# Performance work log

Hardware: AMD Instinct MI355X
Metric: run time of the kernel (lower is better)

The kernel has to match this reference:

```python
import jax, jax.numpy as jnp
import numpy as np

B, L, C = 2, 2048, 1024
H = 16
D = C // H  # 64
MAX_SCALE_MUL = float(np.log(100.0))
EPS = 1e-12


def setup_inputs() -> dict:
    key = jax.random.key(0)
    ks = jax.random.split(key, 6)
    x = jax.random.normal(ks[0], (B, L, C), dtype=jnp.float32)
    attn_bias = jax.random.normal(ks[1], (1, 1, L, L), dtype=jnp.float32) * 0.02
    W_qkv = jax.random.normal(ks[2], (3 * C, C), dtype=jnp.float32) * (1.0 / np.sqrt(C))
    q_bias = jnp.zeros((C,), dtype=jnp.float32)
    v_bias = jnp.zeros((C,), dtype=jnp.float32)
    scale_mul = jnp.full((1, H, 1, 1), np.log(4.0), dtype=jnp.float32)
    W_proj = jax.random.normal(ks[3], (C, C), dtype=jnp.float32) * (1.0 / np.sqrt(C))
    b_proj = jnp.zeros((C,), dtype=jnp.float32)
    return {"x": x, "attn_bias": attn_bias, "W_qkv": W_qkv, "q_bias": q_bias,
            "v_bias": v_bias, "scale_mul": scale_mul, "W_proj": W_proj, "b_proj": b_proj}


def _l2norm(t):
    # F.normalize(dim=-1): x / max(||x||_2, eps)
    n = jnp.sqrt(jnp.sum(t * t, axis=-1, keepdims=True))
    return t / jnp.maximum(n, EPS)


def reference(x, attn_bias, W_qkv, q_bias, v_bias, scale_mul, W_proj, b_proj):
    bias = jnp.concatenate([q_bias, jnp.zeros_like(q_bias), v_bias])  # (3C,)
    qkv = x @ W_qkv.T + bias                     # (B, L, 3C)
    qkv = qkv.reshape(B, L, 3, H, D)
    q, k, v = jnp.moveaxis(qkv, 2, 0)            # each (B, L, H, D)
    q = jnp.transpose(q, (0, 2, 1, 3))           # (B, H, L, D)
    k = jnp.transpose(k, (0, 2, 1, 3))
    v = jnp.transpose(v, (0, 2, 1, 3))
    # attn_l2_norm path: scale = 1, learned per-head scale clamped at log(100)
    sm = jnp.exp(jnp.minimum(scale_mul, MAX_SCALE_MUL))  # (1, H, 1, 1)
    q = _l2norm(q) * sm
    k = _l2norm(k)
    scores = jnp.einsum('bhqd,bhkd->bhqk', q, k) + attn_bias  # scale=1
    attn = jax.nn.softmax(scores, axis=-1)
    out = jnp.einsum('bhqk,bhkd->bhqd', attn, v)  # (B, H, L, D)
    out = jnp.transpose(out, (0, 2, 1, 3)).reshape(B, L, C)
    return out @ W_proj.T + b_proj
```

## Files before the change

### kernel.cpp

```cpp
#include <hip/hip_runtime.h>


typedef __bf16 bf16x8 __attribute__((ext_vector_type(8)));
typedef __bf16 bf16x4 __attribute__((ext_vector_type(4)));
typedef float  f32x4  __attribute__((ext_vector_type(4)));

#define BB 2
#define LL 2048
#define CC 1024
#define HH 16
#define DD 64
#define LOG2E 1.44269504088896f

__device__ __forceinline__ f32x4 mfma_16x16x32(bf16x8 a, bf16x8 b, f32x4 c) {
    return __builtin_amdgcn_mfma_f32_16x16x32_bf16(a, b, c, 0, 0, 0);
}

__device__ __forceinline__ void gload_lds16(const __bf16* g, __bf16* lds) {
    __builtin_amdgcn_global_load_lds(
        (const __attribute__((address_space(1))) unsigned int*)g,
        (__attribute__((address_space(3))) unsigned int*)lds,
        16, 0, 0);
}

__device__ __forceinline__ unsigned pk_bf16(float a, float b) {
    unsigned short ua = __builtin_bit_cast(unsigned short, (__bf16)a);
    unsigned short ub = __builtin_bit_cast(unsigned short, (__bf16)b);
    return (unsigned)ua | ((unsigned)ub << 16);
}

__global__ __launch_bounds__(256) void cvt_bf16_kernel(const float* __restrict__ in,
                                                       __bf16* __restrict__ out, int n4) {
    int i = blockIdx.x * 256 + threadIdx.x;
    if (i >= n4) return;
    float4 v = reinterpret_cast<const float4*>(in)[i];
    bf16x4 o;
    o[0] = (__bf16)v.x; o[1] = (__bf16)v.y; o[2] = (__bf16)v.z; o[3] = (__bf16)v.w;
    reinterpret_cast<bf16x4*>(out)[i] = o;
}

__global__ __launch_bounds__(256) void bias_prep_kernel(const float* __restrict__ bias,
                                                        __bf16* __restrict__ bias_bf) {
    __shared__ float wmax[4];
    const int l = blockIdx.x, tid = threadIdx.x;
    const int w = tid >> 6;
    float4 a = reinterpret_cast<const float4*>(bias + (size_t)l * 2048)[tid];
    float4 b = reinterpret_cast<const float4*>(bias + (size_t)l * 2048 + 1024)[tid];
    float m = fmaxf(fmaxf(fmaxf(a.x, a.y), fmaxf(a.z, a.w)),
                    fmaxf(fmaxf(b.x, b.y), fmaxf(b.z, b.w)));
#pragma unroll
    for (int off = 1; off < 64; off <<= 1) m = fmaxf(m, __shfl_xor(m, off, 64));
    if ((tid & 63) == 0) wmax[w] = m;
    __syncthreads();
    float M = fmaxf(fmaxf(wmax[0], wmax[1]), fmaxf(wmax[2], wmax[3]));
    bf16x4 o0, o1;
    o0[0] = (__bf16)(a.x - M); o0[1] = (__bf16)(a.y - M);
    o0[2] = (__bf16)(a.z - M); o0[3] = (__bf16)(a.w - M);
    o1[0] = (__bf16)(b.x - M); o1[1] = (__bf16)(b.y - M);
    o1[2] = (__bf16)(b.z - M); o1[3] = (__bf16)(b.w - M);
    reinterpret_cast<bf16x4*>(bias_bf + (size_t)l * 2048)[tid] = o0;
    reinterpret_cast<bf16x4*>(bias_bf + (size_t)l * 2048 + 1024)[tid] = o1;
}

template <int OUT_MODE>
__global__ __launch_bounds__(256) void gemm_bt_kernel(
    const __bf16* __restrict__ A, const __bf16* __restrict__ Bm,
    float* __restrict__ Cf, __bf16* __restrict__ Cb,
    const float* __restrict__ bias, int M, int N, int K) {
    __shared__ __bf16 As[128 * 64];
    __shared__ __bf16 Bs[128 * 64];
    const int tid = threadIdx.x;
    const int m0 = blockIdx.x * 128, n0 = blockIdx.y * 128;
    const int w  = tid >> 6, l = tid & 63;
    const int wr = (w >> 1) * 64, wc = (w & 1) * 64;
    const int lr = l & 15, lg = l >> 4;
    const int rmask = (lr & 7) << 4;
    f32x4 acc[4][4] = {};
    const int lrow = l >> 3;
    const int celem = (((l & 7) ^ lrow) << 3);

    for (int kt = 0; kt < K; kt += 64) {
        __syncthreads();
#pragma unroll
        for (int i = 0; i < 4; ++i) {
            const int row = w * 32 + i * 8;
            gload_lds16(A + (size_t)(m0 + row + lrow) * K + kt + celem, &As[row * 64]);
            gload_lds16(Bm + (size_t)(n0 + row + lrow) * K + kt + celem, &Bs[row * 64]);
        }
        asm volatile("s_waitcnt vmcnt(0)" ::: "memory");
        __syncthreads();
#pragma unroll
        for (int kk = 0; kk < 2; ++kk) {
            bf16x8 af[4], bfr[4];
#pragma unroll
            for (int m = 0; m < 4; ++m)
                af[m] = *reinterpret_cast<const bf16x8*>(
                    (char*)As + (wr + m * 16 + lr) * 128 + ((kk * 64 + lg * 16) ^ rmask));
#pragma unroll
            for (int n = 0; n < 4; ++n)
                bfr[n] = *reinterpret_cast<const bf16x8*>(
                    (char*)Bs + (wc + n * 16 + lr) * 128 + ((kk * 64 + lg * 16) ^ rmask));
#pragma unroll
            for (int m = 0; m < 4; ++m)
#pragma unroll
                for (int n = 0; n < 4; ++n)
                    acc[m][n] = mfma_16x16x32(af[m], bfr[n], acc[m][n]);
        }
    }
#pragma unroll
    for (int m = 0; m < 4; ++m) {
#pragma unroll
        for (int n = 0; n < 4; ++n) {
            const int row = m0 + wr + m * 16 + lg * 4;
            const int col = n0 + wc + n * 16 + lr;
#pragma unroll
            for (int r = 0; r < 4; ++r) {
                float v = acc[m][n][r];
                if (OUT_MODE == 0) {
                    Cb[(size_t)(row + r) * N + col] = (__bf16)v;
                } else {
                    Cf[(size_t)(row + r) * N + col] = v + bias[col];
                }
            }
        }
    }
}

__global__ __launch_bounds__(256) void qkv_norm_kernel(
    const __bf16* __restrict__ qkv, const float* __restrict__ q_bias,
    const float* __restrict__ v_bias, const float* __restrict__ scale_mul,
    __bf16* __restrict__ Q, __bf16* __restrict__ K, __bf16* __restrict__ V) {
    const int bl = blockIdx.x;
    const int tid = threadIdx.x;
    const int w = tid >> 6, d = tid & 63;
    const int b = bl >> 11, l = bl & 2047;
    for (int g = w; g < 48; g += 4) {
        const int s = g >> 4, h = g & 15;
        float v = (float)qkv[(size_t)bl * 3072 + g * 64 + d];
        if (s == 0) v += q_bias[h * 64 + d];
        if (s == 2) v += v_bias[h * 64 + d];
        if (s < 2) {
            float ss = v * v;
#pragma unroll
            for (int off = 1; off < 64; off <<= 1) ss += __shfl_xor(ss, off, 64);
            float nrm = sqrtf(ss);
            v = v / fmaxf(nrm, 1e-12f);
            if (s == 0) v *= __expf(fminf(scale_mul[h], 4.60517019f));
        }
        __bf16* dst = (s == 0) ? Q : ((s == 1) ? K : V);
        dst[((size_t)(b * 16 + h) * 2048 + l) * 64 + d] = (__bf16)v;
    }
}

__global__ __launch_bounds__(256) void v_transpose_kernel(const __bf16* __restrict__ Vin,
                                                          __bf16* __restrict__ Vt) {
    __shared__ __bf16 T[64][72];
    const int lb = blockIdx.x, bh = blockIdx.y;
    const int tid = threadIdx.x;
    const size_t base = (size_t)bh * LL * DD;
    const int row = tid >> 2, c = (tid & 3) * 16;
    {
        const __bf16* src = Vin + base + (size_t)(lb * 64 + row) * 64 + c;
        *reinterpret_cast<bf16x8*>(&T[row][c])     = *reinterpret_cast<const bf16x8*>(src);
        *reinterpret_cast<bf16x8*>(&T[row][c + 8]) = *reinterpret_cast<const bf16x8*>(src + 8);
    }
    __syncthreads();
    bf16x8 o0, o1;
#pragma unroll
    for (int j = 0; j < 8; ++j) {
        o0[j] = T[c + j][row];
        o1[j] = T[c + 8 + j][row];
    }
    __bf16* dst = Vt + base + (size_t)row * 2048 + lb * 64 + c;
    *reinterpret_cast<bf16x8*>(dst)     = o0;
    *reinterpret_cast<bf16x8*>(dst + 8) = o1;
}

__global__ __launch_bounds__(256) void attn_kernel(
    const __bf16* __restrict__ Q, const __bf16* __restrict__ K,
    const __bf16* __restrict__ Vt, const __bf16* __restrict__ bias_bf,
    const float* __restrict__ scale_mul, __bf16* __restrict__ Octx) {
    __shared__ __bf16 KVs[2][2][64 * 64];
    const int bh = blockIdx.x, qb = blockIdx.y;
    const int tid = threadIdx.x;
    const int w = tid >> 6, l = tid & 63;
    const int lr = l & 15, lg = l >> 4;
    const int rmask = (lr & 7) << 4;
    const int b = bh >> 4, h = bh & 15;
    const size_t base = (size_t)bh * LL * DD;
    const float smh = __expf(fminf(scale_mul[h], 4.60517019f));
    const float cexp = -smh * LOG2E;

    const int gq = qb * 64 + w * 16 + lr;
    bf16x8 qf[2];
    qf[0] = *reinterpret_cast<const bf16x8*>(Q + base + (size_t)gq * 64 + lg * 8);
    qf[1] = *reinterpret_cast<const bf16x8*>(Q + base + (size_t)gq * 64 + 32 + lg * 8);
    const __bf16* brow = bias_bf + (size_t)gq * 2048;

    const int lrow = l >> 3;
    const int celem = (((l & 7) ^ lrow) << 3);
    auto stage = [&](int buf, int kb) {
        __bf16* Kd = &KVs[buf][0][0];
        __bf16* Vd = &KVs[buf][1][0];
#pragma unroll
        for (int i = 0; i < 2; ++i) {
            const int row = w * 16 + i * 8;
            gload_lds16(K  + base + ((size_t)kb * 64 + row + lrow) * 64 + celem, Kd + row * 64);
            gload_lds16(Vt + base + (size_t)(row + lrow) * 2048 + kb * 64 + celem, Vd + row * 64);
        }
    };

    stage(0, 0);
    asm volatile("s_waitcnt vmcnt(0)" ::: "memory");

    f32x4 Oa[4] = {};
    float lsum = 0.f;
    int cur = 0;
    bf16x4 bcur[4];
#pragma unroll
    for (int t = 0; t < 4; ++t)
        bcur[t] = *reinterpret_cast<const bf16x4*>(brow + t * 16 + lg * 4);

    const int sAx = lr + ((lg & 1) << 5);
    const int sBx = sAx + 16;

    for (int kb = 0; kb < 32; ++kb) {
        __syncthreads();
        if (kb < 31) stage(cur ^ 1, kb + 1);
        bf16x4 bnext[4];
        if (kb < 31) {
#pragma unroll
            for (int t = 0; t < 4; ++t)
                bnext[t] = *reinterpret_cast<const bf16x4*>(brow + (kb + 1) * 64 + t * 16 + lg * 4);
        }

        const char* Kc = (const char*)KVs[cur][0];
        const char* Vc = (const char*)KVs[cur][1];

        f32x4 sa[4] = {};
#pragma unroll
        for (int t = 0; t < 4; ++t) {
            const char* kr = Kc + (t * 16 + lr) * 128;
            bf16x8 kf0 = *reinterpret_cast<const bf16x8*>(kr + ((lg * 16) ^ rmask));
            bf16x8 kf1 = *reinterpret_cast<const bf16x8*>(kr + ((64 + lg * 16) ^ rmask));
            sa[t] = mfma_16x16x32(kf0, qf[0], sa[t]);
            sa[t] = mfma_16x16x32(kf1, qf[1], sa[t]);
        }

        unsigned wv[4][2];
#pragma unroll
        for (int t = 0; t < 4; ++t) {
            float pv[4];
#pragma unroll
            for (int r = 0; r < 4; ++r) {
                float s = sa[t][r] + (float)bcur[t][r];
                pv[r] = exp2f(fmaf(s, LOG2E, cexp));
                lsum += pv[r];
            }
            wv[t][0] = pk_bf16(pv[0], pv[1]);
            wv[t][1] = pk_bf16(pv[2], pv[3]);
        }

        int e0  = __shfl((int)wv[0][0], sAx, 64), e1  = __shfl((int)wv[0][1], sAx, 64);
        int e2  = __shfl((int)wv[0][0], sBx, 64), e3  = __shfl((int)wv[0][1], sBx, 64);
        int e4  = __shfl((int)wv[1][0], sAx, 64), e5  = __shfl((int)wv[1][1], sAx, 64);
        int e6  = __shfl((int)wv[1][0], sBx, 64), e7  = __shfl((int)wv[1][1], sBx, 64);
        int e8  = __shfl((int)wv[2][0], sAx, 64), e9  = __shfl((int)wv[2][1], sAx, 64);
        int e10 = __shfl((int)wv[2][0], sBx, 64), e11 = __shfl((int)wv[2][1], sBx, 64);
        int e12 = __shfl((int)wv[3][0], sAx, 64), e13 = __shfl((int)wv[3][1], sAx, 64);
        int e14 = __shfl((int)wv[3][0], sBx, 64), e15 = __shfl((int)wv[3][1], sBx, 64);
        const bool hi2 = (lg & 2) != 0;
        union Upa { unsigned u[4]; bf16x8 v; } pa0, pa1;
        pa0.u[0] = hi2 ? (unsigned)e4  : (unsigned)e0;
        pa0.u[1] = hi2 ? (unsigned)e5  : (unsigned)e1;
        pa0.u[2] = hi2 ? (unsigned)e6  : (unsigned)e2;
        pa0.u[3] = hi2 ? (unsigned)e7  : (unsigned)e3;
        pa1.u[0] = hi2 ? (unsigned)e12 : (unsigned)e8;
        pa1.u[1] = hi2 ? (unsigned)e13 : (unsigned)e9;
        pa1.u[2] = hi2 ? (unsigned)e14 : (unsigned)e10;
        pa1.u[3] = hi2 ? (unsigned)e15 : (unsigned)e11;

#pragma unroll
        for (int t = 0; t < 4; ++t) {
            const char* vr = Vc + (t * 16 + lr) * 128;
            bf16x8 vf0 = *reinterpret_cast<const bf16x8*>(vr + ((lg * 16) ^ rmask));
            bf16x8 vf1 = *reinterpret_cast<const bf16x8*>(vr + ((64 + lg * 16) ^ rmask));
            Oa[t] = mfma_16x16x32(pa0.v, vf0, Oa[t]);
            Oa[t] = mfma_16x16x32(pa1.v, vf1, Oa[t]);
        }

        if (kb < 31) {
            asm volatile("s_waitcnt vmcnt(0)" ::: "memory");
#pragma unroll
            for (int t = 0; t < 4; ++t) bcur[t] = bnext[t];
        }
        cur ^= 1;
    }

    lsum += __shfl_xor(lsum, 16, 64);
    lsum += __shfl_xor(lsum, 32, 64);
    float inv[4];
#pragma unroll
    for (int r = 0; r < 4; ++r) inv[r] = 1.0f / __shfl(lsum, lg * 4 + r, 64);

#pragma unroll
    for (int t = 0; t < 4; ++t)
#pragma unroll
        for (int r = 0; r < 4; ++r) {
            const int row = qb * 64 + w * 16 + lg * 4 + r;
            float o = Oa[t][r] * inv[r];
            Octx[((size_t)(b * 2048 + row)) * 1024 + h * 64 + t * 16 + lr] = (__bf16)o;
        }
}

extern "C" void kernel_launch(void* const* d_in, const int* in_sizes, int n_in,
                              void* d_out, int out_size, void* d_ws, size_t ws_size,
                              hipStream_t stream) {
    const float* x         = (const float*)d_in[0];
    const float* attn_bias = (const float*)d_in[1];
    const float* W_qkv     = (const float*)d_in[2];
    const float* q_bias    = (const float*)d_in[3];
    const float* v_bias    = (const float*)d_in[4];
    const float* scale_mul = (const float*)d_in[5];
    const float* W_proj    = (const float*)d_in[6];
    const float* b_proj    = (const float*)d_in[7];
    float* out = (float*)d_out;

    char* ws = (char*)d_ws;
    size_t off = 0;
    auto alloc = [&](size_t bytes) {
        void* p = ws + off;
        off = (off + bytes + 255) & ~(size_t)255;
        return p;
    };
    __bf16* xb     = (__bf16*)alloc((size_t)4096 * 1024 * 2);
    __bf16* wqkvb  = (__bf16*)alloc((size_t)3072 * 1024 * 2);
    __bf16* wprojb = (__bf16*)alloc((size_t)1024 * 1024 * 2);
    __bf16* qkvb   = (__bf16*)alloc((size_t)4096 * 3072 * 2);
    __bf16* Qw     = (__bf16*)alloc((size_t)BB * HH * LL * DD * 2);
    __bf16* Kw     = (__bf16*)alloc((size_t)BB * HH * LL * DD * 2);
    __bf16* Vw     = (__bf16*)alloc((size_t)BB * HH * LL * DD * 2);
    __bf16* Oc     = (__bf16*)alloc((size_t)4096 * 1024 * 2);
    __bf16* bias_bf = qkvb;
    __bf16* Vt      = qkvb + (size_t)2048 * 2048;

    cvt_bf16_kernel<<<4096, 256, 0, stream>>>(x, xb, 4096 * 1024 / 4);
    cvt_bf16_kernel<<<3072, 256, 0, stream>>>(W_qkv, wqkvb, 3072 * 1024 / 4);
    cvt_bf16_kernel<<<1024, 256, 0, stream>>>(W_proj, wprojb, 1024 * 1024 / 4);

    gemm_bt_kernel<0><<<dim3(32, 24), 256, 0, stream>>>(
        xb, wqkvb, nullptr, qkvb, nullptr, 4096, 3072, 1024);

    qkv_norm_kernel<<<4096, 256, 0, stream>>>(qkvb, q_bias, v_bias, scale_mul, Qw, Kw, Vw);

    bias_prep_kernel<<<2048, 256, 0, stream>>>(attn_bias, bias_bf);
    v_transpose_kernel<<<dim3(32, 32), 256, 0, stream>>>(Vw, Vt);

    attn_kernel<<<dim3(32, 32), 256, 0, stream>>>(Qw, Kw, Vt, bias_bf, scale_mul, Oc);

    gemm_bt_kernel<1><<<dim3(32, 8), 256, 0, stream>>>(
        Oc, wprojb, out, nullptr, b_proj, 4096, 1024, 1024);
}
```

Measured before the change: 200.5 us.

## Load K/V fragments directly from global and pass P through LDS

Drops the double-buffered LDS staging of K and V tiles along with the block barriers. Each wave now loads its K and V MFMA fragments straight from global memory, relying on L2/cache reuse across waves and blocks. The P transpose no longer uses 16 cross-lane shuffles; it is written to a small per-wave swizzled LDS tile and read back. The change also remaps block indices with a swizzle for better L2 locality and adds a launch_bounds occupancy hint. The risk is redundant global traffic, since each of the four waves fetches the same K/V, and exposed global-load latency without explicit prefetch.

```diff
diff --git a/kernel.cpp b/kernel.cpp
--- a/kernel.cpp
+++ b/kernel.cpp
@@ -21,12 +21,6 @@
         (const __attribute__((address_space(1))) unsigned int*)g,
         (__attribute__((address_space(3))) unsigned int*)lds,
         16, 0, 0);
-}
-
-__device__ __forceinline__ unsigned pk_bf16(float a, float b) {
-    unsigned short ua = __builtin_bit_cast(unsigned short, (__bf16)a);
-    unsigned short ub = __builtin_bit_cast(unsigned short, (__bf16)b);
-    return (unsigned)ua | ((unsigned)ub << 16);
 }
 
 __global__ __launch_bounds__(256) void cvt_bf16_kernel(const float* __restrict__ in,
@@ -176,13 +170,15 @@
     *reinterpret_cast<bf16x8*>(dst + 8) = o1;
 }
 
-__global__ __launch_bounds__(256) void attn_kernel(
+__global__ __launch_bounds__(256, 4) void attn_kernel(
     const __bf16* __restrict__ Q, const __bf16* __restrict__ K,
     const __bf16* __restrict__ Vt, const __bf16* __restrict__ bias_bf,
     const float* __restrict__ scale_mul, __bf16* __restrict__ Octx) {
-    __shared__ __bf16 KVs[2][2][64 * 64];
-    const int bh = blockIdx.x, qb = blockIdx.y;
+    __shared__ __bf16 Ps[64 * 64];
     const int tid = threadIdx.x;
+    const int flat = blockIdx.x + (blockIdx.y << 5);
+    const int swz  = (flat & 7) * 128 + (flat >> 3);
+    const int bh = swz >> 5, qb = swz & 31;
     const int w = tid >> 6, l = tid & 63;
     const int lr = l & 15, lg = l >> 4;
     const int rmask = (lr & 7) << 4;
@@ -197,36 +193,33 @@
     qf[1] = *reinterpret_cast<const bf16x8*>(Q + base + (size_t)gq * 64 + 32 + lg * 8);
     const __bf16* brow = bias_bf + (size_t)gq * 2048;
 
-    const int lrow = l >> 3;
-    const int celem = (((l & 7) ^ lrow) << 3);
-    auto stage = [&](int buf, int kb) {
-        __bf16* Kd = &KVs[buf][0][0];
-        __bf16* Vd = &KVs[buf][1][0];
-#pragma unroll
-        for (int i = 0; i < 2; ++i) {
-            const int row = w * 16 + i * 8;
-            gload_lds16(K  + base + ((size_t)kb * 64 + row + lrow) * 64 + celem, Kd + row * 64);
-            gload_lds16(Vt + base + (size_t)(row + lrow) * 2048 + kb * 64 + celem, Vd + row * 64);
-        }
-    };
-
-    stage(0, 0);
-    asm volatile("s_waitcnt vmcnt(0)" ::: "memory");
+    const __bf16* Kp = K  + base + (size_t)lr * 64 + lg * 8;
+    const __bf16* Vp = Vt + base + (size_t)lr * 2048 + lg * 8;
 
     f32x4 Oa[4] = {};
     float lsum = 0.f;
-    int cur = 0;
+    char* psb = (char*)Ps + (w * 16 + lr) * 128;
+
     bf16x4 bcur[4];
 #pragma unroll
     for (int t = 0; t < 4; ++t)
         bcur[t] = *reinterpret_cast<const bf16x4*>(brow + t * 16 + lg * 4);
 
-    const int sAx = lr + ((lg & 1) << 5);
-    const int sBx = sAx + 16;
-
     for (int kb = 0; kb < 32; ++kb) {
-        __syncthreads();
-        if (kb < 31) stage(cur ^ 1, kb + 1);
+        bf16x8 kf0[4], kf1[4];
+#pragma unroll
+        for (int t = 0; t < 4; ++t) {
+            const __bf16* kr = Kp + (size_t)(kb * 64 + t * 16) * 64;
+            kf0[t] = *reinterpret_cast<const bf16x8*>(kr);
+            kf1[t] = *reinterpret_cast<const bf16x8*>(kr + 32);
+        }
+        f32x4 sa[4] = {};
+#pragma unroll
+        for (int t = 0; t < 4; ++t) {
+            sa[t] = mfma_16x16x32(kf0[t], qf[0], sa[t]);
+            sa[t] = mfma_16x16x32(kf1[t], qf[1], sa[t]);
+        }
+
         bf16x4 bnext[4];
         if (kb < 31) {
 #pragma unroll
@@ -234,67 +227,40 @@
                 bnext[t] = *reinterpret_cast<const bf16x4*>(brow + (kb + 1) * 64 + t * 16 + lg * 4);
         }
 
-        const char* Kc = (const char*)KVs[cur][0];
-        const char* Vc = (const char*)KVs[cur][1];
-
-        f32x4 sa[4] = {};
-#pragma unroll
-        for (int t = 0; t < 4; ++t) {
-            const char* kr = Kc + (t * 16 + lr) * 128;
-            bf16x8 kf0 = *reinterpret_cast<const bf16x8*>(kr + ((lg * 16) ^ rmask));
-            bf16x8 kf1 = *reinterpret_cast<const bf16x8*>(kr + ((64 + lg * 16) ^ rmask));
-            sa[t] = mfma_16x16x32(kf0, qf[0], sa[t]);
-            sa[t] = mfma_16x16x32(kf1, qf[1], sa[t]);
-        }
-
-        unsigned wv[4][2];
-#pragma unroll
-        for (int t = 0; t < 4; ++t) {
-            float pv[4];
+#pragma unroll
+        for (int t = 0; t < 4; ++t) {
+            bf16x4 pb;
 #pragma unroll
             for (int r = 0; r < 4; ++r) {
                 float s = sa[t][r] + (float)bcur[t][r];
-                pv[r] = exp2f(fmaf(s, LOG2E, cexp));
-                lsum += pv[r];
+                float p = exp2f(fmaf(s, LOG2E, cexp));
+                lsum += p;
+                pb[r] = (__bf16)p;
             }
-            wv[t][0] = pk_bf16(pv[0], pv[1]);
-            wv[t][1] = pk_bf16(pv[2], pv[3]);
-        }
-
-        int e0  = __shfl((int)wv[0][0], sAx, 64), e1  = __shfl((int)wv[0][1], sAx, 64);
-        int e2  = __shfl((int)wv[0][0], sBx, 64), e3  = __shfl((int)wv[0][1], sBx, 64);
-        int e4  = __shfl((int)wv[1][0], sAx, 64), e5  = __shfl((int)wv[1][1], sAx, 64);
-        int e6  = __shfl((int)wv[1][0], sBx, 64), e7  = __shfl((int)wv[1][1], sBx, 64);
-        int e8  = __shfl((int)wv[2][0], sAx, 64), e9  = __shfl((int)wv[2][1], sAx, 64);
-        int e10 = __shfl((int)wv[2][0], sBx, 64), e11 = __shfl((int)wv[2][1], sBx, 64);
-        int e12 = __shfl((int)wv[3][0], sAx, 64), e13 = __shfl((int)wv[3][1], sAx, 64);
-        int e14 = __shfl((int)wv[3][0], sBx, 64), e15 = __shfl((int)wv[3][1], sBx, 64);
-        const bool hi2 = (lg & 2) != 0;
-        union Upa { unsigned u[4]; bf16x8 v; } pa0, pa1;
-        pa0.u[0] = hi2 ? (unsigned)e4  : (unsigned)e0;
-        pa0.u[1] = hi2 ? (unsigned)e5  : (unsigned)e1;
-        pa0.u[2] = hi2 ? (unsigned)e6  : (unsigned)e2;
-        pa0.u[3] = hi2 ? (unsigned)e7  : (unsigned)e3;
-        pa1.u[0] = hi2 ? (unsigned)e12 : (unsigned)e8;
-        pa1.u[1] = hi2 ? (unsigned)e13 : (unsigned)e9;
-        pa1.u[2] = hi2 ? (unsigned)e14 : (unsigned)e10;
-        pa1.u[3] = hi2 ? (unsigned)e15 : (unsigned)e11;
-
-#pragma unroll
-        for (int t = 0; t < 4; ++t) {
-            const char* vr = Vc + (t * 16 + lr) * 128;
-            bf16x8 vf0 = *reinterpret_cast<const bf16x8*>(vr + ((lg * 16) ^ rmask));
-            bf16x8 vf1 = *reinterpret_cast<const bf16x8*>(vr + ((64 + lg * 16) ^ rmask));
-            Oa[t] = mfma_16x16x32(pa0.v, vf0, Oa[t]);
-            Oa[t] = mfma_16x16x32(pa1.v, vf1, Oa[t]);
+            *reinterpret_cast<bf16x4*>(psb + ((t * 32 + lg * 8) ^ rmask)) = pb;
+        }
+
+        bf16x8 vf0[4], vf1[4];
+#pragma unroll
+        for (int t = 0; t < 4; ++t) {
+            const __bf16* vr = Vp + (size_t)(t * 16) * 2048 + kb * 64;
+            vf0[t] = *reinterpret_cast<const bf16x8*>(vr);
+            vf1[t] = *reinterpret_cast<const bf16x8*>(vr + 32);
+        }
+
+        bf16x8 pf0 = *reinterpret_cast<const bf16x8*>(psb + ((lg * 16) ^ rmask));
+        bf16x8 pf1 = *reinterpret_cast<const bf16x8*>(psb + ((64 + lg * 16) ^ rmask));
+
+#pragma unroll
+        for (int t = 0; t < 4; ++t) {
+            Oa[t] = mfma_16x16x32(pf0, vf0[t], Oa[t]);
+            Oa[t] = mfma_16x16x32(pf1, vf1[t], Oa[t]);
         }
 
         if (kb < 31) {
-            asm volatile("s_waitcnt vmcnt(0)" ::: "memory");
 #pragma unroll
             for (int t = 0; t < 4; ++t) bcur[t] = bnext[t];
         }
-        cur ^= 1;
     }
 
     lsum += __shfl_xor(lsum, 16, 64);
```

New measurement: 384.2 us. 1.92x slower.
